# Kernel tuning notes

Hardware: AMD Instinct MI355X
Metric: run time of the kernel (lower is better)

The kernel has to match this reference:

```python
import jax, jax.numpy as jnp
import numpy as np

B, T_ENC, IN, H, TGT = 128, 128, 3, 512, 32

def setup_inputs() -> dict:
    key = jax.random.key(0)
    ks = jax.random.split(key, 16)
    s = 0.05
    return {
        "x": jax.random.normal(ks[0], (B, T_ENC, IN), jnp.float32),
        "y": jax.random.normal(ks[1], (B, TGT, 1), jnp.float32),
        # encoder: 2 layers x 2 directions (dim0 = [fwd, bwd])
        "enc_Wih0": jax.random.normal(ks[2], (2, H, IN), jnp.float32) * s,
        "enc_Whh0": jax.random.normal(ks[3], (2, H, H), jnp.float32) * s,
        "enc_Wih1": jax.random.normal(ks[4], (2, H, 2 * H), jnp.float32) * s,
        "enc_Whh1": jax.random.normal(ks[5], (2, H, H), jnp.float32) * s,
        "enc_bih": jax.random.normal(ks[6], (2, 2, H), jnp.float32) * s,  # (layer, dir, H)
        "enc_bhh": jax.random.normal(ks[7], (2, 2, H), jnp.float32) * s,
        # decoder: 4-layer unidirectional stack (matches hn shape (4,B,H))
        "dec_Wih0": jax.random.normal(ks[8], (H, IN), jnp.float32) * s,
        "dec_Wihr": jax.random.normal(ks[9], (3, H, H), jnp.float32) * s,
        "dec_Whh": jax.random.normal(ks[10], (4, H, H), jnp.float32) * s,
        "dec_bih": jax.random.normal(ks[11], (4, H), jnp.float32) * s,
        "dec_bhh": jax.random.normal(ks[12], (4, H), jnp.float32) * s,
        "lin_W": jax.random.normal(ks[13], (1, H), jnp.float32) * s,
        "lin_b": jax.random.normal(ks[14], (1,), jnp.float32) * s,
        "target_len": TGT,
        "teacher_forcing_ratio": 0,
    }

def _rnn_dir(x, Wih, Whh, bih, bhh, reverse):
    # x: (B,T,I) -> outputs (B,T,H), final carry (B,H)
    xs = jnp.einsum('bti,hi->tbh', x, Wih) + bih  # precompute input projection
    def step(h, xt):
        h = jnp.tanh(xt + h @ Whh.T + bhh)
        return h, h
    h0 = jnp.zeros((x.shape[0], Whh.shape[0]), x.dtype)
    hT, ys = jax.lax.scan(step, h0, xs, reverse=reverse)
    return jnp.transpose(ys, (1, 0, 2)), hT

def _forward(x, y, enc_Wih0, enc_Whh0, enc_Wih1, enc_Whh1, enc_bih, enc_bhh,
             dec_Wih0, dec_Wihr, dec_Whh, dec_bih, dec_bhh, lin_W, lin_b,
             target_len, teacher_forcing_ratio):
    # ---- bidirectional encoder, 2 layers ----
    of0, hf0 = _rnn_dir(x, enc_Wih0[0], enc_Whh0[0], enc_bih[0, 0], enc_bhh[0, 0], False)
    ob0, hb0 = _rnn_dir(x, enc_Wih0[1], enc_Whh0[1], enc_bih[0, 1], enc_bhh[0, 1], True)
    l0 = jnp.concatenate([of0, ob0], axis=-1)  # (B,T,2H)
    of1, hf1 = _rnn_dir(l0, enc_Wih1[0], enc_Whh1[0], enc_bih[1, 0], enc_bhh[1, 0], False)
    ob1, hb1 = _rnn_dir(l0, enc_Wih1[1], enc_Whh1[1], enc_bih[1, 1], enc_bhh[1, 1], True)
    hn = jnp.stack([hf0, hb0, hf1, hb1])  # (4,B,H), torch layer/dir ordering

    dec_in0 = x[:, -1, :]  # (B,IN)

    def dec_step(carry, _):
        hs, xin = carry
        inp = xin
        new_hs = []
        for l in range(4):
            Wih = dec_Wih0 if l == 0 else dec_Wihr[l - 1]
            h = jnp.tanh(inp @ Wih.T + dec_bih[l] + hs[l] @ dec_Whh[l].T + dec_bhh[l])
            new_hs.append(h)
            inp = h
        out = inp @ lin_W.T + lin_b  # (B,1)
        o0 = out[:, 0]
        s1 = xin[:, 0] - o0
        s2 = xin[:, 1] - s1
        nxt = jnp.stack([o0, s1, s2], axis=1)  # (B,3)
        return (jnp.stack(new_hs), nxt), out

    _, outs = jax.lax.scan(dec_step, (hn, dec_in0), None, length=target_len)
    return jnp.transpose(outs, (1, 0, 2))  # (B, target_len, 1)

def reference(x, y, enc_Wih0, enc_Whh0, enc_Wih1, enc_Whh1, enc_bih, enc_bhh,
              dec_Wih0, dec_Wihr, dec_Whh, dec_bih, dec_bhh, lin_W, lin_b,
              target_len, teacher_forcing_ratio):
    return _forward(x, y, enc_Wih0, enc_Whh0, enc_Wih1, enc_Whh1, enc_bih, enc_bhh,
                    dec_Wih0, dec_Wihr, dec_Whh, dec_bih, dec_bhh, lin_W, lin_b,
                    target_len, teacher_forcing_ratio)
```

## Files before the change

kernel.cpp:

```cpp
#include <hip/hip_runtime.h>
#include <cmath>

#define B 128
#define T 128
#define H 512
#define TGT 32

#define SCOPE_AGENT __HIP_MEMORY_SCOPE_AGENT

struct Args {
  const float *x, *eWih0, *eWhh0, *eWih1, *eWhh1, *ebih, *ebhh;
  const float *dWih0, *dWihr, *dWhh, *dbih, *dbhh, *linW, *linb;
  float *dst;
  float *xing;
  float *l0;
  unsigned *ctr;
  float *out;
};

__global__ void kinit(float* __restrict__ st, unsigned* __restrict__ ctr) {
  int idx = blockIdx.x * 256 + threadIdx.x;
  for (int i = idx; i < 4 * B * H; i += 256 * 256) st[i] = 0.f;
  if (idx < 64) ctr[idx] = 0u;
}

__device__ __forceinline__ void bumpR(unsigned* c) {
  __syncthreads();
  if (threadIdx.x == 0)
    __hip_atomic_fetch_add(c, 1u, __ATOMIC_RELAXED, SCOPE_AGENT);
}
__device__ __forceinline__ void waitcR(unsigned* c, unsigned tgt) {
  if (threadIdx.x == 0)
    while (__hip_atomic_load(c, __ATOMIC_RELAXED, SCOPE_AGENT) < tgt)
      __builtin_amdgcn_s_sleep(2);
  __syncthreads();
}
__device__ __forceinline__ void bumpF(unsigned* c) {
  __syncthreads();
  if (threadIdx.x == 0)
    __hip_atomic_fetch_add(c, 1u, __ATOMIC_RELEASE, SCOPE_AGENT);
}
__device__ __forceinline__ void waitcF(unsigned* c, unsigned tgt) {
  if (threadIdx.x == 0) {
    while (__hip_atomic_load(c, __ATOMIC_RELAXED, SCOPE_AGENT) < tgt)
      __builtin_amdgcn_s_sleep(2);
    __builtin_amdgcn_fence(__ATOMIC_ACQUIRE, "agent");
  }
  __syncthreads();
}

__device__ __forceinline__ void stC(float* p, float v) {
  __hip_atomic_store(p, v, __ATOMIC_RELAXED, SCOPE_AGENT);
}
__device__ __forceinline__ float ldC(const float* p) {
  return __hip_atomic_load(p, __ATOMIC_RELAXED, SCOPE_AGENT);
}

template <int ROWLEN, int GSTRIDE>
__device__ __forceinline__ void stage(const float* __restrict__ g,
                                      float* __restrict__ l, int rows, int lstride) {
  int total = rows * ROWLEN;
  for (int idx = (int)threadIdx.x * 4; idx < total; idx += 1024) {
    int r = idx / ROWLEN, k = idx - r * ROWLEN;
    float4 v = *(const float4*)(g + (size_t)r * GSTRIDE + k);
    *(float4*)(l + r * lstride + k) = v;
  }
}

__device__ __forceinline__ void stage16(const float* __restrict__ g,
                                        float* __restrict__ l) {
  const int t = threadIdx.x;
  const int r0 = t >> 7, k0 = (t & 127) * 4;
  float4 v[8];
#pragma unroll
  for (int i = 0; i < 8; i++)
    v[i] = *(const float4*)(g + (size_t)(r0 + 2 * i) * 512 + k0);
#pragma unroll
  for (int i = 0; i < 8; i++)
    *(float4*)(l + (r0 + 2 * i) * 516 + k0) = v[i];
}

__device__ __forceinline__ void stageC16(const float* __restrict__ g,
                                         float* __restrict__ l) {
  const unsigned long long* gu = (const unsigned long long*)g;
  unsigned long long* lu = (unsigned long long*)l;
  const int t = threadIdx.x;
  unsigned long long v[16];
#pragma unroll
  for (int i = 0; i < 16; i++)
    v[i] = __hip_atomic_load(gu + (size_t)i * 256 + t, __ATOMIC_RELAXED, SCOPE_AGENT);
#pragma unroll
  for (int i = 0; i < 16; i++)
    lu[i * 258 + t] = v[i];
}

#define DOT4(accv, hv, wv) accv += hv.x*wv.x + hv.y*wv.y + hv.z*wv.z + hv.w*wv.w
#define DOT4B(accv, hv, wv, iv, uv)                                       \
  accv += hv.x*wv.x + hv.y*wv.y + hv.z*wv.z + hv.w*wv.w                   \
        + iv.x*uv.x + iv.y*uv.y + iv.z*uv.z + iv.w*uv.w

__device__ __forceinline__ float dotK16(const float* hb, const float* wb, int kg) {
  float acc[4][4];
#pragma unroll
  for (int rr = 0; rr < 4; rr++)
#pragma unroll
    for (int cc = 0; cc < 4; cc++) acc[rr][cc] = 0.f;
#pragma unroll
  for (int i = 0; i < 8; i++) {
    const int k = i * 64;
    float4 h0 = *(const float4*)(hb + k);
    float4 h1 = *(const float4*)(hb + 516 + k);
    float4 h2 = *(const float4*)(hb + 1032 + k);
    float4 h3 = *(const float4*)(hb + 1548 + k);
    float4 w0 = *(const float4*)(wb + k);
    float4 w1 = *(const float4*)(wb + 516 + k);
    float4 w2 = *(const float4*)(wb + 1032 + k);
    float4 w3 = *(const float4*)(wb + 1548 + k);
    DOT4(acc[0][0],h0,w0); DOT4(acc[0][1],h0,w1); DOT4(acc[0][2],h0,w2); DOT4(acc[0][3],h0,w3);
    DOT4(acc[1][0],h1,w0); DOT4(acc[1][1],h1,w1); DOT4(acc[1][2],h1,w2); DOT4(acc[1][3],h1,w3);
    DOT4(acc[2][0],h2,w0); DOT4(acc[2][1],h2,w1); DOT4(acc[2][2],h2,w2); DOT4(acc[2][3],h2,w3);
    DOT4(acc[3][0],h3,w0); DOT4(acc[3][1],h3,w1); DOT4(acc[3][2],h3,w2); DOT4(acc[3][3],h3,w3);
  }
#pragma unroll
  for (int rr = 0; rr < 4; rr++)
#pragma unroll
    for (int cc = 0; cc < 4; cc++) {
      float v = acc[rr][cc];
      v += __shfl_xor(v, 1); v += __shfl_xor(v, 2);
      v += __shfl_xor(v, 4); v += __shfl_xor(v, 8);
      acc[rr][cc] = v;
    }
  float sv = 0.f;
#pragma unroll
  for (int rr = 0; rr < 4; rr++)
#pragma unroll
    for (int cc = 0; cc < 4; cc++)
      sv = (kg == rr * 4 + cc) ? acc[rr][cc] : sv;
  return sv;
}

__global__ __launch_bounds__(256, 1) void birnn_all(Args a) {
  __shared__ __align__(16) float sm[33088];
  const int tid = threadIdx.x;
  const int bx = blockIdx.x;

  {
    const int pt = bx & 7, ntile = bx >> 3;
    const int b0 = pt * 16, n0 = ntile * 16;
    const int kg = tid & 15, ni = (tid >> 4) & 3, bi = tid >> 6;
    float* wl0 = sm;
    float* wl1 = sm + 8256;
    float* hl0 = sm + 16512;
    float* hl1 = sm + 24768;
    unsigned* cF = a.ctr + pt;
    unsigned* cB = a.ctr + 8 + pt;

    stage16(a.eWhh0 + (size_t)n0 * H, wl0);
    stage16(a.eWhh0 + (size_t)(H + n0) * H, wl1);

    const int nlane = n0 + ni * 4 + (kg & 3);
    const int rloc  = bi * 4 + (kg >> 2);
    float gwf0 = a.eWih0[(0 * H + nlane) * 3 + 0];
    float gwf1 = a.eWih0[(0 * H + nlane) * 3 + 1];
    float gwf2 = a.eWih0[(0 * H + nlane) * 3 + 2];
    float gwb0 = a.eWih0[(1 * H + nlane) * 3 + 0];
    float gwb1 = a.eWih0[(1 * H + nlane) * 3 + 1];
    float gwb2 = a.eWih0[(1 * H + nlane) * 3 + 2];
    float bf = a.ebih[nlane] + a.ebhh[nlane];
    float bb = a.ebih[H + nlane] + a.ebhh[H + nlane];
    const int hoff = bi * 4 * 516 + kg * 4;
    const int woff = ni * 4 * 516 + kg * 4;

    for (int s = 0; s < T; s++) {
      int tf = s, tb = T - 1 - s;
      const float* xrf = a.x + ((size_t)(b0 + rloc) * T + tf) * 3;
      const float* xrb = a.x + ((size_t)(b0 + rloc) * T + tb) * 3;
      float af = bf + xrf[0] * gwf0 + xrf[1] * gwf1 + xrf[2] * gwf2;
      float ab = bb + xrb[0] * gwb0 + xrb[1] * gwb1 + xrb[2] * gwb2;

      if (s) waitcR(cF, 32u * s); else __syncthreads();
      stageC16(a.dst + ((size_t)((s & 1) * 4 + 0) * B + b0) * H, hl0);
      __syncthreads();
      float of = tanhf(af + dotK16(hl0 + hoff, wl0 + woff, kg));
      stC(a.dst + ((size_t)(((s + 1) & 1) * 4 + 0) * B + (b0 + rloc)) * H + nlane, of);
      bumpR(cF);
      a.l0[((size_t)tf * B + (b0 + rloc)) * 1024 + nlane] = of;

      if (s) waitcR(cB, 32u * s);
      stageC16(a.dst + ((size_t)((s & 1) * 4 + 1) * B + b0) * H, hl1);
      __syncthreads();
      float ob = tanhf(ab + dotK16(hl1 + hoff, wl1 + woff, kg));
      stC(a.dst + ((size_t)(((s + 1) & 1) * 4 + 1) * B + (b0 + rloc)) * H + nlane, ob);
      bumpR(cB);
      a.l0[((size_t)tb * B + (b0 + rloc)) * 1024 + H + nlane] = ob;
    }
  }
  { unsigned* g = a.ctr + 48; bumpF(g); waitcF(g, 256u); }

  {
    float* xl = sm;
    float* wl = sm + 16448;
    const int kg = tid & 3;
    const int ci = (tid >> 2) & 15;
    const int ri = tid >> 6;
    for (int rt = 0; rt < 4; rt++) {
      int row0 = (bx * 4 + rt) * 16;
      __syncthreads();
      stage<1024, 1024>(a.l0 + (size_t)row0 * 1024, xl, 16, 1028);
      __syncthreads();
      for (int nc = 0; nc < 16; nc++) {
        const int nb = nc * 64 + ci * 4 + kg;
        float biasv = a.ebih[(2 + (nb >> 9)) * H + (nb & 511)] +
                      a.ebhh[(2 + (nb >> 9)) * H + (nb & 511)];
        float acc[4][4];
#pragma unroll
        for (int rr = 0; rr < 4; rr++)
#pragma unroll
          for (int cc = 0; cc < 4; cc++) acc[rr][cc] = 0.f;

        for (int kp = 0; kp < 4; kp++) {
          __syncthreads();
          stage<256, 1024>(a.eWih1 + (size_t)(nc * 64) * 1024 + kp * 256, wl, 64, 260);
          __syncthreads();
          const float* xp0 = xl + (ri * 4 + 0) * 1028 + kp * 256 + kg * 4;
          const float* xp1 = xp0 + 1028;
          const float* xp2 = xp0 + 2 * 1028;
          const float* xp3 = xp0 + 3 * 1028;
          const float* wq0 = wl + (ci * 4 + 0) * 260 + kg * 4;
          const float* wq1 = wq0 + 260;
          const float* wq2 = wq0 + 2 * 260;
          const float* wq3 = wq0 + 3 * 260;
#pragma unroll 4
          for (int i = 0; i < 16; i++) {
            const int k = i * 16;
            float4 x0 = *(const float4*)(xp0 + k);
            float4 x1 = *(const float4*)(xp1 + k);
            float4 x2 = *(const float4*)(xp2 + k);
            float4 x3 = *(const float4*)(xp3 + k);
            float4 w0 = *(const float4*)(wq0 + k);
            float4 w1 = *(const float4*)(wq1 + k);
            float4 w2 = *(const float4*)(wq2 + k);
            float4 w3 = *(const float4*)(wq3 + k);
            DOT4(acc[0][0], x0, w0); DOT4(acc[0][1], x0, w1); DOT4(acc[0][2], x0, w2); DOT4(acc[0][3], x0, w3);
            DOT4(acc[1][0], x1, w0); DOT4(acc[1][1], x1, w1); DOT4(acc[1][2], x1, w2); DOT4(acc[1][3], x1, w3);
            DOT4(acc[2][0], x2, w0); DOT4(acc[2][1], x2, w1); DOT4(acc[2][2], x2, w2); DOT4(acc[2][3], x2, w3);
            DOT4(acc[3][0], x3, w0); DOT4(acc[3][1], x3, w1); DOT4(acc[3][2], x3, w2); DOT4(acc[3][3], x3, w3);
          }
        }
#pragma unroll
        for (int rr = 0; rr < 4; rr++)
#pragma unroll
          for (int cc = 0; cc < 4; cc++) {
            float v = acc[rr][cc];
            v += __shfl_xor(v, 1); v += __shfl_xor(v, 2);
            acc[rr][cc] = v;
          }
        float o0 = 0.f, o1 = 0.f, o2 = 0.f, o3 = 0.f;
#pragma unroll
        for (int cc = 0; cc < 4; cc++) {
          o0 = (kg == cc) ? acc[0][cc] : o0;
          o1 = (kg == cc) ? acc[1][cc] : o1;
          o2 = (kg == cc) ? acc[2][cc] : o2;
          o3 = (kg == cc) ? acc[3][cc] : o3;
        }
        float* gr = a.l0 + (size_t)(row0 + ri * 4) * 1024 + nb;
        gr[0]        = o0 + biasv;
        gr[1024]     = o1 + biasv;
        gr[2 * 1024] = o2 + biasv;
        gr[3 * 1024] = o3 + biasv;
      }
    }
  }
  { unsigned* g = a.ctr + 48; bumpF(g); waitcF(g, 512u); }

  {
    const int pt = bx & 7, ntile = bx >> 3;
    const int b0 = pt * 16, n0 = ntile * 16;
    const int kg = tid & 15, ni = (tid >> 4) & 3, bi = tid >> 6;
    float* wl0 = sm;
    float* wl1 = sm + 8256;
    float* hl0 = sm + 16512;
    float* hl1 = sm + 24768;
    unsigned* cF = a.ctr + 16 + pt;
    unsigned* cB = a.ctr + 24 + pt;

    stage16(a.eWhh1 + (size_t)n0 * H, wl0);
    stage16(a.eWhh1 + (size_t)(H + n0) * H, wl1);

    const int nlane = n0 + ni * 4 + (kg & 3);
    const int rloc  = bi * 4 + (kg >> 2);
    const int hoff = bi * 4 * 516 + kg * 4;
    const int woff = ni * 4 * 516 + kg * 4;

    for (int s = 0; s < T; s++) {
      int tf = s, tb = T - 1 - s;
      float af = a.l0[((size_t)tf * B + (b0 + rloc)) * 1024 + nlane];
      float ab = a.l0[((size_t)tb * B + (b0 + rloc)) * 1024 + H + nlane];

      if (s) waitcR(cF, 32u * s); else __syncthreads();
      stageC16(a.dst + ((size_t)((s & 1) * 4 + 2) * B + b0) * H, hl0);
      __syncthreads();
      float of = tanhf(af + dotK16(hl0 + hoff, wl0 + woff, kg));
      stC(a.dst + ((size_t)(((s + 1) & 1) * 4 + 2) * B + (b0 + rloc)) * H + nlane, of);
      bumpR(cF);

      if (s) waitcR(cB, 32u * s);
      stageC16(a.dst + ((size_t)((s & 1) * 4 + 3) * B + b0) * H, hl1);
      __syncthreads();
      float ob = tanhf(ab + dotK16(hl1 + hoff, wl1 + woff, kg));
      stC(a.dst + ((size_t)(((s + 1) & 1) * 4 + 3) * B + (b0 + rloc)) * H + nlane, ob);
      bumpR(cB);
    }
  }
  { unsigned* g = a.ctr + 48; bumpF(g); waitcF(g, 768u); }

  {
    const int btile = bx & 7, ntile = bx >> 3;
    const int b0 = btile * 16, n0 = ntile * 16;
    const int j = tid & 15, bl = tid >> 4;
    const int kg = tid & 15;
    const int ni = (tid >> 4) & 3;
    const int bi = tid >> 6;
    float* whh  = sm;
    float* wir  = sm + 8256;
    float* hlc  = sm + 16512;
    float* hin  = sm + 24768;
    float* xinL = sm + 33024;
    unsigned* c = a.ctr + 32 + btile;

    const int nlane = n0 + ni * 4 + (kg & 3);
    const int rloc  = bi * 4 + (kg >> 2);
    float w00 = a.dWih0[nlane * 3 + 0], w01 = a.dWih0[nlane * 3 + 1], w02 = a.dWih0[nlane * 3 + 2];
    float bias0 = a.dbih[0 * H + nlane] + a.dbhh[0 * H + nlane];
    float bias1 = a.dbih[1 * H + nlane] + a.dbhh[1 * H + nlane];
    float bias2 = a.dbih[2 * H + nlane] + a.dbhh[2 * H + nlane];
    float bias3 = a.dbih[3 * H + nlane] + a.dbhh[3 * H + nlane];

    const float* hp0 = hlc + (bi * 4 + 0) * 516 + kg * 4;
    const float* hp1 = hp0 + 516;
    const float* hp2 = hp0 + 2 * 516;
    const float* hp3 = hp0 + 3 * 516;
    const float* ip0 = hin + (bi * 4 + 0) * 516 + kg * 4;
    const float* ip1 = ip0 + 516;
    const float* ip2 = ip0 + 2 * 516;
    const float* ip3 = ip0 + 3 * 516;
    const float* wp0 = whh + (ni * 4 + 0) * 516 + kg * 4;
    const float* wp1 = wp0 + 516;
    const float* wp2 = wp0 + 2 * 516;
    const float* wp3 = wp0 + 3 * 516;
    const float* up0 = wir + (ni * 4 + 0) * 516 + kg * 4;
    const float* up1 = up0 + 516;
    const float* up2 = up0 + 2 * 516;
    const float* up3 = up0 + 3 * 516;

    stage16(a.dWhh + (size_t)(0 * H + n0) * H, whh);
    stageC16(a.dst + ((size_t)(0 * 4 + 0) * B + b0) * H, hlc);

    for (int m = 0; m < 128; m++) {
      int s = m >> 2, l = m & 3;
      int p = s & 1, q = 1 - p;
      if (m) waitcR(c, 32u * m); else __syncthreads();

      if (l) {
        stageC16(a.dst + ((size_t)(q * 4 + (l - 1)) * B + b0) * H, hin);
      } else if (s) {
        stageC16(a.dst + ((size_t)(p * 4 + 3) * B + b0) * H, hin);
      }
      __syncthreads();

      if (l == 0) {
        if (s == 0) {
          if (j == 0) {
            const float* xr = a.x + ((size_t)(b0 + bl) * T + (T - 1)) * 3;
            float v0 = xr[0], v1 = xr[1], v2 = xr[2];
            xinL[bl * 4 + 0] = v0; xinL[bl * 4 + 1] = v1; xinL[bl * 4 + 2] = v2;
            if (ntile == 0) {
              float* xw = a.xing + (size_t)(b0 + bl) * 4;
              stC(xw + 0, v0); stC(xw + 1, v1); stC(xw + 2, v2);
            }
          }
        } else {
          const float* h3r = hin + bl * 516;
          float v = 0.f;
          for (int k = j; k < H; k += 16) v += h3r[k] * a.linW[k];
          v += __shfl_xor(v, 8); v += __shfl_xor(v, 4);
          v += __shfl_xor(v, 2); v += __shfl_xor(v, 1);
          float o0 = v + a.linb[0];
          const float* xp = a.xing + ((size_t)((s - 1) & 1) * B + (b0 + bl)) * 4;
          float sv1 = ldC(xp + 0) - o0;
          float sv2 = ldC(xp + 1) - sv1;
          if (j == 0) {
            xinL[bl * 4 + 0] = o0; xinL[bl * 4 + 1] = sv1; xinL[bl * 4 + 2] = sv2;
            if (ntile == 0) {
              float* xw = a.xing + ((size_t)(s & 1) * B + (b0 + bl)) * 4;
              stC(xw + 0, o0); stC(xw + 1, sv1); stC(xw + 2, sv2);
              a.out[(size_t)(b0 + bl) * TGT + (s - 1)] = o0;
            }
          }
        }
        __syncthreads();
      }

      float acc[4][4];
#pragma unroll
      for (int rr = 0; rr < 4; rr++)
#pragma unroll
        for (int cc = 0; cc < 4; cc++) acc[rr][cc] = 0.f;

      if (l) {
#pragma unroll 2
        for (int i = 0; i < 8; i++) {
          const int k = i * 64;
          float4 h0 = *(const float4*)(hp0 + k);
          float4 h1 = *(const float4*)(hp1 + k);
          float4 h2 = *(const float4*)(hp2 + k);
          float4 h3 = *(const float4*)(hp3 + k);
          float4 i0 = *(const float4*)(ip0 + k);
          float4 i1 = *(const float4*)(ip1 + k);
          float4 i2 = *(const float4*)(ip2 + k);
          float4 i3 = *(const float4*)(ip3 + k);
          float4 w0 = *(const float4*)(wp0 + k);
          float4 w1 = *(const float4*)(wp1 + k);
          float4 w2 = *(const float4*)(wp2 + k);
          float4 w3 = *(const float4*)(wp3 + k);
          float4 u0 = *(const float4*)(up0 + k);
          float4 u1 = *(const float4*)(up1 + k);
          float4 u2 = *(const float4*)(up2 + k);
          float4 u3 = *(const float4*)(up3 + k);
          DOT4B(acc[0][0], h0, w0, i0, u0); DOT4B(acc[0][1], h0, w1, i0, u1);
          DOT4B(acc[0][2], h0, w2, i0, u2); DOT4B(acc[0][3], h0, w3, i0, u3);
          DOT4B(acc[1][0], h1, w0, i1, u0); DOT4B(acc[1][1], h1, w1, i1, u1);
          DOT4B(acc[1][2], h1, w2, i1, u2); DOT4B(acc[1][3], h1, w3, i1, u3);
          DOT4B(acc[2][0], h2, w0, i2, u0); DOT4B(acc[2][1], h2, w1, i2, u1);
          DOT4B(acc[2][2], h2, w2, i2, u2); DOT4B(acc[2][3], h2, w3, i2, u3);
          DOT4B(acc[3][0], h3, w0, i3, u0); DOT4B(acc[3][1], h3, w1, i3, u1);
          DOT4B(acc[3][2], h3, w2, i3, u2); DOT4B(acc[3][3], h3, w3, i3, u3);
        }
      } else {
#pragma unroll 2
        for (int i = 0; i < 8; i++) {
          const int k = i * 64;
          float4 h0 = *(const float4*)(hp0 + k);
          float4 h1 = *(const float4*)(hp1 + k);
          float4 h2 = *(const float4*)(hp2 + k);
          float4 h3 = *(const float4*)(hp3 + k);
          float4 w0 = *(const float4*)(wp0 + k);
          float4 w1 = *(const float4*)(wp1 + k);
          float4 w2 = *(const float4*)(wp2 + k);
          float4 w3 = *(const float4*)(wp3 + k);
          DOT4(acc[0][0], h0, w0); DOT4(acc[0][1], h0, w1); DOT4(acc[0][2], h0, w2); DOT4(acc[0][3], h0, w3);
          DOT4(acc[1][0], h1, w0); DOT4(acc[1][1], h1, w1); DOT4(acc[1][2], h1, w2); DOT4(acc[1][3], h1, w3);
          DOT4(acc[2][0], h2, w0); DOT4(acc[2][1], h2, w1); DOT4(acc[2][2], h2, w2); DOT4(acc[2][3], h2, w3);
          DOT4(acc[3][0], h3, w0); DOT4(acc[3][1], h3, w1); DOT4(acc[3][2], h3, w2); DOT4(acc[3][3], h3, w3);
        }
      }
#pragma unroll
      for (int rr = 0; rr < 4; rr++)
#pragma unroll
        for (int cc = 0; cc < 4; cc++) {
          float v = acc[rr][cc];
          v += __shfl_xor(v, 1); v += __shfl_xor(v, 2);
          v += __shfl_xor(v, 4); v += __shfl_xor(v, 8);
          acc[rr][cc] = v;
        }
      float sv = 0.f;
#pragma unroll
      for (int rr = 0; rr < 4; rr++)
#pragma unroll
        for (int cc = 0; cc < 4; cc++)
          sv = (kg == rr * 4 + cc) ? acc[rr][cc] : sv;

      float bs = (l == 0) ? bias0 : (l == 1) ? bias1 : (l == 2) ? bias2 : bias3;
      float at = bs;
      if (l == 0)
        at += xinL[rloc * 4 + 0] * w00 + xinL[rloc * 4 + 1] * w01 + xinL[rloc * 4 + 2] * w02;
      float hnew = tanhf(at + sv);
      stC(a.dst + ((size_t)(q * 4 + l) * B + (b0 + rloc)) * H + nlane, hnew);
      bumpR(c);

      if (m < 127) {
        int m2 = m + 1, l2 = m2 & 3, s2 = m2 >> 2, p2 = s2 & 1;
        stage16(a.dWhh + (size_t)(l2 * H + n0) * H, whh);
        if (l2)
          stage16(a.dWihr + (size_t)((l2 - 1) * H + n0) * H, wir);
        stageC16(a.dst + ((size_t)(p2 * 4 + l2) * B + b0) * H, hlc);
      }
    }

    if (ntile == 0) {
      waitcR(c, 32u * 128);
      const float* h3g = a.dst + ((size_t)(0 * 4 + 3) * B + (b0 + bl)) * H;
      float v = 0.f;
      for (int k = j; k < H; k += 16) v += ldC(h3g + k) * a.linW[k];
      v += __shfl_xor(v, 8); v += __shfl_xor(v, 4);
      v += __shfl_xor(v, 2); v += __shfl_xor(v, 1);
      if (j == 0) a.out[(size_t)(b0 + bl) * TGT + 31] = v + a.linb[0];
    }
  }
}

#undef DOT4
#undef DOT4B

extern "C" void kernel_launch(void* const* d_in, const int* in_sizes, int n_in,
                              void* d_out, int out_size, void* d_ws, size_t ws_size,
                              hipStream_t stream) {
  float* dst  = (float*)d_ws;
  float* xing = dst + 2 * 4 * B * H;
  unsigned* ctr = (unsigned*)((char*)d_ws + 2101248);
  float* l0 = (float*)((char*)d_ws + 2101504);

  kinit<<<256, 256, 0, stream>>>(dst, ctr);

  Args args;
  args.x     = (const float*)d_in[0];
  args.eWih0 = (const float*)d_in[2];
  args.eWhh0 = (const float*)d_in[3];
  args.eWih1 = (const float*)d_in[4];
  args.eWhh1 = (const float*)d_in[5];
  args.ebih  = (const float*)d_in[6];
  args.ebhh  = (const float*)d_in[7];
  args.dWih0 = (const float*)d_in[8];
  args.dWihr = (const float*)d_in[9];
  args.dWhh  = (const float*)d_in[10];
  args.dbih  = (const float*)d_in[11];
  args.dbhh  = (const float*)d_in[12];
  args.linW  = (const float*)d_in[13];
  args.linb  = (const float*)d_in[14];
  args.dst = dst; args.xing = xing; args.l0 = l0; args.ctr = ctr;
  args.out = (float*)d_out;

  void* kp[] = { &args };
  hipLaunchCooperativeKernel((void*)birnn_all, dim3(256), dim3(256), kp, 0, stream);
}
```

Baseline: 5.706 ms.

## Split encoder recurrence work by direction across blocks with half-batch ping-pong groups

Reassigns the encoder recurrent phases so each block handles one direction (dirE) with a 32-wide hidden tile and two 8-row batch groups, instead of both directions with 16-wide tiles and 16-row batches. Each block stages half as much hidden state per sync (stageC8), and each counter group now has 16 producers. The counters are reused across layers by offsetting the wait target. The aim is to cut per-step staging traffic and let the two batch groups interleave so sync waits overlap with compute. The risk is more blocks contending on each counter and a different load balance across the step.

```diff
diff --git a/kernel.cpp b/kernel.cpp
--- a/kernel.cpp
+++ b/kernel.cpp
@@ -91,6 +91,20 @@
     v[i] = __hip_atomic_load(gu + (size_t)i * 256 + t, __ATOMIC_RELAXED, SCOPE_AGENT);
 #pragma unroll
   for (int i = 0; i < 16; i++)
+    lu[i * 258 + t] = v[i];
+}
+
+__device__ __forceinline__ void stageC8(const float* __restrict__ g,
+                                        float* __restrict__ l) {
+  const unsigned long long* gu = (const unsigned long long*)g;
+  unsigned long long* lu = (unsigned long long*)l;
+  const int t = threadIdx.x;
+  unsigned long long v[8];
+#pragma unroll
+  for (int i = 0; i < 8; i++)
+    v[i] = __hip_atomic_load(gu + (size_t)i * 256 + t, __ATOMIC_RELAXED, SCOPE_AGENT);
+#pragma unroll
+  for (int i = 0; i < 8; i++)
     lu[i * 258 + t] = v[i];
 }
 
@@ -144,55 +158,51 @@
   const int tid = threadIdx.x;
   const int bx = blockIdx.x;
 
+  const int dirE = bx >> 7, prE = (bx >> 4) & 7, ntE = bx & 15;
+  const int b0A = prE * 8, b0B = prE * 8 + 64, n0E = ntE * 32;
+  const int kgE = tid & 15, niE = (tid >> 4) & 7, biE = tid >> 7;
+  const int nlaneE = n0E + niE * 4 + (kgE & 3);
+  const int rlocE  = biE * 4 + (kgE >> 2);
+  const int hoffE = biE * 4 * 516 + kgE * 4;
+  const int woffE = niE * 4 * 516 + kgE * 4;
+
   {
-    const int pt = bx & 7, ntile = bx >> 3;
-    const int b0 = pt * 16, n0 = ntile * 16;
-    const int kg = tid & 15, ni = (tid >> 4) & 3, bi = tid >> 6;
-    float* wl0 = sm;
-    float* wl1 = sm + 8256;
-    float* hl0 = sm + 16512;
-    float* hl1 = sm + 24768;
-    unsigned* cF = a.ctr + pt;
-    unsigned* cB = a.ctr + 8 + pt;
-
-    stage16(a.eWhh0 + (size_t)n0 * H, wl0);
-    stage16(a.eWhh0 + (size_t)(H + n0) * H, wl1);
-
-    const int nlane = n0 + ni * 4 + (kg & 3);
-    const int rloc  = bi * 4 + (kg >> 2);
-    float gwf0 = a.eWih0[(0 * H + nlane) * 3 + 0];
-    float gwf1 = a.eWih0[(0 * H + nlane) * 3 + 1];
-    float gwf2 = a.eWih0[(0 * H + nlane) * 3 + 2];
-    float gwb0 = a.eWih0[(1 * H + nlane) * 3 + 0];
-    float gwb1 = a.eWih0[(1 * H + nlane) * 3 + 1];
-    float gwb2 = a.eWih0[(1 * H + nlane) * 3 + 2];
-    float bf = a.ebih[nlane] + a.ebhh[nlane];
-    float bb = a.ebih[H + nlane] + a.ebhh[H + nlane];
-    const int hoff = bi * 4 * 516 + kg * 4;
-    const int woff = ni * 4 * 516 + kg * 4;
+    float* wl  = sm;
+    float* hlA = sm + 16512;
+    float* hlB = sm + 20640;
+    unsigned* cA = a.ctr + dirE * 16 + prE;
+    unsigned* cB = a.ctr + dirE * 16 + prE + 8;
+
+    stage16(a.eWhh0 + (size_t)(dirE * H + n0E) * H, wl);
+    stage16(a.eWhh0 + (size_t)(dirE * H + n0E + 16) * H, wl + 16 * 516);
+
+    float wx0 = a.eWih0[(dirE * H + nlaneE) * 3 + 0];
+    float wx1 = a.eWih0[(dirE * H + nlaneE) * 3 + 1];
+    float wx2 = a.eWih0[(dirE * H + nlaneE) * 3 + 2];
+    float bias = a.ebih[dirE * H + nlaneE] + a.ebhh[dirE * H + nlaneE];
 
     for (int s = 0; s < T; s++) {
-      int tf = s, tb = T - 1 - s;
-      const float* xrf = a.x + ((size_t)(b0 + rloc) * T + tf) * 3;
-      const float* xrb = a.x + ((size_t)(b0 + rloc) * T + tb) * 3;
-      float af = bf + xrf[0] * gwf0 + xrf[1] * gwf1 + xrf[2] * gwf2;
-      float ab = bb + xrb[0] * gwb0 + xrb[1] * gwb1 + xrb[2] * gwb2;
-
-      if (s) waitcR(cF, 32u * s); else __syncthreads();
-      stageC16(a.dst + ((size_t)((s & 1) * 4 + 0) * B + b0) * H, hl0);
-      __syncthreads();
-      float of = tanhf(af + dotK16(hl0 + hoff, wl0 + woff, kg));
-      stC(a.dst + ((size_t)(((s + 1) & 1) * 4 + 0) * B + (b0 + rloc)) * H + nlane, of);
-      bumpR(cF);
-      a.l0[((size_t)tf * B + (b0 + rloc)) * 1024 + nlane] = of;
-
-      if (s) waitcR(cB, 32u * s);
-      stageC16(a.dst + ((size_t)((s & 1) * 4 + 1) * B + b0) * H, hl1);
-      __syncthreads();
-      float ob = tanhf(ab + dotK16(hl1 + hoff, wl1 + woff, kg));
-      stC(a.dst + ((size_t)(((s + 1) & 1) * 4 + 1) * B + (b0 + rloc)) * H + nlane, ob);
+      int t_ = dirE ? (T - 1 - s) : s;
+      const float* xrA = a.x + ((size_t)(b0A + rlocE) * T + t_) * 3;
+      const float* xrB = a.x + ((size_t)(b0B + rlocE) * T + t_) * 3;
+      float aA = bias + xrA[0] * wx0 + xrA[1] * wx1 + xrA[2] * wx2;
+      float aB = bias + xrB[0] * wx0 + xrB[1] * wx1 + xrB[2] * wx2;
+
+      if (s) waitcR(cA, 16u * s); else __syncthreads();
+      stageC8(a.dst + ((size_t)((s & 1) * 4 + dirE) * B + b0A) * H, hlA);
+      __syncthreads();
+      float oA = tanhf(aA + dotK16(hlA + hoffE, wl + woffE, kgE));
+      stC(a.dst + ((size_t)(((s + 1) & 1) * 4 + dirE) * B + (b0A + rlocE)) * H + nlaneE, oA);
+      bumpR(cA);
+      a.l0[((size_t)t_ * B + (b0A + rlocE)) * 1024 + dirE * H + nlaneE] = oA;
+
+      if (s) waitcR(cB, 16u * s);
+      stageC8(a.dst + ((size_t)((s & 1) * 4 + dirE) * B + b0B) * H, hlB);
+      __syncthreads();
+      float oB = tanhf(aB + dotK16(hlB + hoffE, wl + woffE, kgE));
+      stC(a.dst + ((size_t)(((s + 1) & 1) * 4 + dirE) * B + (b0B + rlocE)) * H + nlaneE, oB);
       bumpR(cB);
-      a.l0[((size_t)tb * B + (b0 + rloc)) * 1024 + H + nlane] = ob;
+      a.l0[((size_t)t_ * B + (b0B + rlocE)) * 1024 + dirE * H + nlaneE] = oB;
     }
   }
   { unsigned* g = a.ctr + 48; bumpF(g); waitcF(g, 256u); }
@@ -274,41 +284,33 @@
   { unsigned* g = a.ctr + 48; bumpF(g); waitcF(g, 512u); }
 
   {
-    const int pt = bx & 7, ntile = bx >> 3;
-    const int b0 = pt * 16, n0 = ntile * 16;
-    const int kg = tid & 15, ni = (tid >> 4) & 3, bi = tid >> 6;
-    float* wl0 = sm;
-    float* wl1 = sm + 8256;
-    float* hl0 = sm + 16512;
-    float* hl1 = sm + 24768;
-    unsigned* cF = a.ctr + 16 + pt;
-    unsigned* cB = a.ctr + 24 + pt;
-
-    stage16(a.eWhh1 + (size_t)n0 * H, wl0);
-    stage16(a.eWhh1 + (size_t)(H + n0) * H, wl1);
-
-    const int nlane = n0 + ni * 4 + (kg & 3);
-    const int rloc  = bi * 4 + (kg >> 2);
-    const int hoff = bi * 4 * 516 + kg * 4;
-    const int woff = ni * 4 * 516 + kg * 4;
+    float* wl  = sm;
+    float* hlA = sm + 16512;
+    float* hlB = sm + 20640;
+    unsigned* cA = a.ctr + dirE * 16 + prE;
+    unsigned* cB = a.ctr + dirE * 16 + prE + 8;
+    const unsigned base = 16u * T;
+
+    stage16(a.eWhh1 + (size_t)(dirE * H + n0E) * H, wl);
+    stage16(a.eWhh1 + (size_t)(dirE * H + n0E + 16) * H, wl + 16 * 516);
 
     for (int s = 0; s < T; s++) {
-      int tf = s, tb = T - 1 - s;
-      float af = a.l0[((size_t)tf * B + (b0 + rloc)) * 1024 + nlane];
-      float ab = a.l0[((size_t)tb * B + (b0 + rloc)) * 1024 + H + nlane];
-
-      if (s) waitcR(cF, 32u * s); else __syncthreads();
-      stageC16(a.dst + ((size_t)((s & 1) * 4 + 2) * B + b0) * H, hl0);
-      __syncthreads();
-      float of = tanhf(af + dotK16(hl0 + hoff, wl0 + woff, kg));
-      stC(a.dst + ((size_t)(((s + 1) & 1) * 4 + 2) * B + (b0 + rloc)) * H + nlane, of);
-      bumpR(cF);
-
-      if (s) waitcR(cB, 32u * s);
-      stageC16(a.dst + ((size_t)((s & 1) * 4 + 3) * B + b0) * H, hl1);
-      __syncthreads();
-      float ob = tanhf(ab + dotK16(hl1 + hoff, wl1 + woff, kg));
-      stC(a.dst + ((size_t)(((s + 1) & 1) * 4 + 3) * B + (b0 + rloc)) * H + nlane, ob);
+      int t_ = dirE ? (T - 1 - s) : s;
+      float aA = a.l0[((size_t)t_ * B + (b0A + rlocE)) * 1024 + dirE * H + nlaneE];
+      float aB = a.l0[((size_t)t_ * B + (b0B + rlocE)) * 1024 + dirE * H + nlaneE];
+
+      if (s) waitcR(cA, base + 16u * s); else __syncthreads();
+      stageC8(a.dst + ((size_t)((s & 1) * 4 + 2 + dirE) * B + b0A) * H, hlA);
+      __syncthreads();
+      float oA = tanhf(aA + dotK16(hlA + hoffE, wl + woffE, kgE));
+      stC(a.dst + ((size_t)(((s + 1) & 1) * 4 + 2 + dirE) * B + (b0A + rlocE)) * H + nlaneE, oA);
+      bumpR(cA);
+
+      if (s) waitcR(cB, base + 16u * s);
+      stageC8(a.dst + ((size_t)((s & 1) * 4 + 2 + dirE) * B + b0B) * H, hlB);
+      __syncthreads();
+      float oB = tanhf(aB + dotK16(hlB + hoffE, wl + woffE, kgE));
+      stC(a.dst + ((size_t)(((s + 1) & 1) * 4 + 2 + dirE) * B + (b0B + rlocE)) * H + nlaneE, oB);
       bumpR(cB);
     }
   }
```

Result: slower. 7.864 ms (+37.8%).
